# Optimization experiments

Hardware: AMD Instinct MI355X
Metric: run time of the kernel (lower is better)

## Reference

```python
import jax, jax.numpy as jnp
import numpy as np

B, T, D_MODEL, N_HEADS = 2, 2048, 2048, 16
D_HEAD = D_MODEL // N_HEADS
SCALE = 1.0 / np.sqrt(D_HEAD)


def setup_inputs() -> dict:
    key = jax.random.key(0)
    ks = jax.random.split(key, 5)
    w_std = 1.0 / np.sqrt(D_MODEL)
    x = jax.random.normal(ks[0], (B, T, D_MODEL), dtype=jnp.float32)
    W_q = jax.random.normal(ks[1], (D_MODEL, D_MODEL), dtype=jnp.float32) * w_std
    W_k = jax.random.normal(ks[2], (D_MODEL, D_MODEL), dtype=jnp.float32) * w_std
    W_v = jax.random.normal(ks[3], (D_MODEL, D_MODEL), dtype=jnp.float32) * w_std
    W_o = jax.random.normal(ks[4], (D_MODEL, D_MODEL), dtype=jnp.float32) * w_std
    return {"x": x, "W_q": W_q, "W_k": W_k, "W_v": W_v, "W_o": W_o}


def _split_heads(y):
    # [B, T, D] -> [B, H, T, d_head]
    b, t, _ = y.shape
    return y.reshape(b, t, N_HEADS, D_HEAD).transpose(0, 2, 1, 3)


def reference(x, W_q, W_k, W_v, W_o):
    # Linear layers (torch nn.Linear: y = x @ W.T)
    Q = _split_heads(x @ W_q.T)
    K = _split_heads(x @ W_k.T)
    V = _split_heads(x @ W_v.T)
    # Causal softmax attention (math-equivalent to the tiled online-softmax loop)
    scores = jnp.einsum('bhqd,bhkd->bhqk', Q, K) * SCALE
    causal_mask = jnp.tril(jnp.ones((T, T), dtype=bool))  # [T, T]
    scores = jnp.where(causal_mask, scores, -jnp.inf)
    P = jax.nn.softmax(scores, axis=-1)
    O = jnp.einsum('bhqk,bhkd->bhqd', P, V)
    out = O.transpose(0, 2, 1, 3).reshape(B, T, D_MODEL)  # merge heads
    return out @ W_o.T
```

## Files before the change

kernel.cpp:

```cpp
#include <hip/hip_runtime.h>
#include <hip/hip_bf16.h>
#include <hip/hip_fp16.h>

#define B_   2
#define T_   2048
#define DM   2048
#define NH   16
#define DH   128
#define M_   (B_*T_)
#define SCALE_ 0.08838834764831845f

typedef _Float16 f16;
typedef f16  half8 __attribute__((ext_vector_type(8)));
typedef f16  half4 __attribute__((ext_vector_type(4)));
typedef float f32x4 __attribute__((ext_vector_type(4)));

#define GL16(gp, lp) __builtin_amdgcn_global_load_lds( \
    (const __attribute__((address_space(1))) void*)(gp), \
    (__attribute__((address_space(3))) void*)(lp), 16, 0, 0)

#define MFMA16(a, b, c) __builtin_amdgcn_mfma_f32_16x16x32_f16((a), (b), (c), 0, 0, 0)

struct CvtArgs { const float* s[5]; f16* d[5]; };

__global__ __launch_bounds__(256) void convert_all(CvtArgs a) {
    size_t i4 = (size_t)blockIdx.x * 256 + threadIdx.x;
    int r; size_t off;
    if (i4 < 2097152) { r = 0; off = i4; }
    else { size_t k = i4 - 2097152; r = 1 + (int)(k >> 20); off = k & 1048575; }
    float4 v = *((const float4*)a.s[r] + off);
    half4 h;
    h[0] = (f16)v.x; h[1] = (f16)v.y; h[2] = (f16)v.z; h[3] = (f16)v.w;
    *((half4*)a.d[r] + off) = h;
}

#define NT_K 32

__global__ __launch_bounds__(512, 2)
void qkv3(const f16* __restrict__ A, const f16* __restrict__ Bw,
          f16* __restrict__ dst)
{
    __shared__ __align__(16) char smem[114688];

    const int tid  = threadIdx.x;
    const int lane = tid & 63;
    const int w    = tid >> 6;
    const int wr   = w >> 1, wc = w & 1;

    const int id = (blockIdx.x & 7) * 64 + (blockIdx.x >> 3);
    const int bm = id & 15, bn = id >> 4;
    const int m0 = bm * 256, n0 = bn * 192;

    const int scol8 = (((tid & 7) ^ ((tid >> 3) & 7)) << 3);
    const int rc0 = (((lane >> 4) * 16)      ) ^ ((lane & 7) << 4);
    const int rc1 = (64 + (lane >> 4) * 16   ) ^ ((lane & 7) << 4);

    f32x4 acc[4][6] = {};

#define QSTAGE_A(bufb, ch, s, kt) GL16( \
    A + (size_t)(m0 + (ch)*128 + (tid>>8)*64 + (s)*32 + ((tid>>3)&31)) * 2048 + (kt)*64 + scol8, \
    smem + (bufb)*57344 + (ch)*16384 + (s)*8192 + w*1024)
#define QSTAGE_B(bufb, u, kt) GL16( \
    Bw + (size_t)(n0 + (tid>>7)*48 + (u)*16 + ((tid>>3)&15)) * 2048 + (kt)*64 + scol8, \
    smem + (bufb)*57344 + 32768 + (u)*8192 + w*1024)

    const int abase = (wr >> 1) * 16384 + (wr & 1) * 4096 + (lane & 15) * 128;
    const int bbase = 32768 + wc * 4096 + (lane & 15) * 128;

    half8 af0[4][2], af1[4][2], bnx[2];

    QSTAGE_A(0, 0, 0, 0); QSTAGE_A(0, 0, 1, 0);
    QSTAGE_A(0, 1, 0, 0); QSTAGE_A(0, 1, 1, 0);
    QSTAGE_B(0, 0, 0);    QSTAGE_B(0, 1, 0);    QSTAGE_B(0, 2, 0);
    {
        asm volatile("s_waitcnt vmcnt(2)" ::: "memory");
        __builtin_amdgcn_s_barrier();
        __builtin_amdgcn_sched_barrier(0);
        const char* buf0 = smem;
        #pragma unroll
        for (int m = 0; m < 4; ++m) {
            const char* p = buf0 + (m >> 1) * 8192 + abase + (m & 1) * 2048;
            af0[m][0] = *(const half8*)(p + rc0);
            af0[m][1] = *(const half8*)(p + rc1);
        }
        bnx[0] = *(const half8*)(buf0 + bbase + rc0);
        bnx[1] = *(const half8*)(buf0 + bbase + rc1);
    }

#define GATE(n_) do { \
    asm volatile("s_waitcnt vmcnt(" #n_ ")" ::: "memory"); \
    __builtin_amdgcn_s_barrier(); \
    __builtin_amdgcn_sched_barrier(0); \
} while (0)

#define MFC(AF, BB, f_) do { \
    __builtin_amdgcn_s_setprio(1); \
    _Pragma("unroll") \
    for (int m_ = 0; m_ < 4; ++m_) { \
        acc[m_][f_] = MFMA16(AF[m_][0], (BB)[0], acc[m_][f_]); \
        acc[m_][f_] = MFMA16(AF[m_][1], (BB)[1], acc[m_][f_]); \
    } \
    __builtin_amdgcn_s_setprio(0); \
} while (0)

#define RDB(dstv, off) do { \
    const char* p_ = buf + bbase + (off); \
    dstv[0] = *(const half8*)(p_ + rc0); \
    dstv[1] = *(const half8*)(p_ + rc1); \
} while (0)

#define BODY(t_, c_, AFC, AFN) do { \
    const char* buf  = smem + (c_) * 57344; \
    const char* nbuf = smem + ((c_) ^ 1) * 57344; \
    const int  kt    = ((t_) + 1 < NT_K) ? (t_) + 1 : (t_); \
    half8 b3[2], b1[2], b4[2], b2[2], b5[2]; \
     \
    RDB(b3, 2048); \
    QSTAGE_A((c_) ^ 1, 0, 0, kt); QSTAGE_A((c_) ^ 1, 0, 1, kt); \
    MFC(AFC, bnx, 0); \
     \
    GATE(3); \
    RDB(b1, 8192); \
    QSTAGE_A((c_) ^ 1, 1, 0, kt); QSTAGE_A((c_) ^ 1, 1, 1, kt); \
    MFC(AFC, b3, 3); \
     \
    RDB(b4, 8192 + 2048); \
    QSTAGE_B((c_) ^ 1, 0, kt); \
    MFC(AFC, b1, 1); \
     \
    GATE(5); \
    RDB(b2, 16384); \
    QSTAGE_B((c_) ^ 1, 1, kt); \
    MFC(AFC, b4, 4); \
     \
    GATE(1); \
    RDB(b5, 16384 + 2048); \
    { const char* p_ = nbuf + abase; \
      AFN[0][0] = *(const half8*)(p_ + rc0); \
      AFN[0][1] = *(const half8*)(p_ + rc1); \
      AFN[1][0] = *(const half8*)(p_ + 2048 + rc0); \
      AFN[1][1] = *(const half8*)(p_ + 2048 + rc1); } \
    QSTAGE_B((c_) ^ 1, 2, kt); \
    MFC(AFC, b2, 2); \
     \
    { const char* p_ = nbuf + 8192 + abase; \
      AFN[2][0] = *(const half8*)(p_ + rc0); \
      AFN[2][1] = *(const half8*)(p_ + rc1); \
      AFN[3][0] = *(const half8*)(p_ + 2048 + rc0); \
      AFN[3][1] = *(const half8*)(p_ + 2048 + rc1); } \
    { const char* p_ = nbuf + bbase; \
      bnx[0] = *(const half8*)(p_ + rc0); \
      bnx[1] = *(const half8*)(p_ + rc1); } \
    MFC(AFC, b5, 5); \
} while (0)

    for (int t = 0; t < NT_K; t += 2) {
        BODY(t,     0, af0, af1);
        BODY(t + 1, 1, af1, af0);
    }
#undef BODY
#undef RDB
#undef MFC
#undef GATE
#undef QSTAGE_A
#undef QSTAGE_B

    asm volatile("s_waitcnt vmcnt(0)" ::: "memory");

    #pragma unroll
    for (int m = 0; m < 4; ++m)
        #pragma unroll
        for (int f = 0; f < 6; ++f)
            #pragma unroll
            for (int j = 0; j < 4; ++j) {
                int row  = m0 + wr * 64 + m * 16 + (lane >> 4) * 4 + j;
                int gcol = n0 + wc * 96 + f * 16 + (lane & 15);
                int sec = gcol >> 11, cic = gcol & 2047;
                int b = row >> 11, tt = row & (T_ - 1);
                int h = cic >> 7, d = cic & 127;
                float cs = (sec == 0) ? SCALE_ : 1.0f;
                dst[(size_t)sec * ((size_t)M_ * 2048) +
                    ((size_t)(b * NH + h) * T_ + tt) * DH + d] = (f16)(acc[m][f][j] * cs);
            }
}

__global__ __launch_bounds__(512, 4)
void wo2(const f16* __restrict__ A, const f16* __restrict__ Bw,
         float* __restrict__ Cf)
{
    __shared__ __align__(16) char smem[65536];

    const int tid  = threadIdx.x;
    const int lane = tid & 63;
    const int w    = tid >> 6;
    const int wr   = w >> 2, wc = w & 3;

    const int id = (blockIdx.x & 7) * 64 + (blockIdx.x >> 3);
    const int bm = id & 31, bn = id >> 5;
    const int m0 = bm * 128, n0 = bn * 128;

    const int scol8 = (((tid & 7) ^ ((tid >> 3) & 7)) << 3);
    const int rc0 = (((lane >> 4) * 16)      ) ^ ((lane & 7) << 4);
    const int rc1 = (64 + (lane >> 4) * 16   ) ^ ((lane & 7) << 4);

    f32x4 acc[4][2] = {};

#define WSTAGE_A(bufb, s, kt) GL16( \
    A + (size_t)(m0 + (tid>>8)*64 + (s)*32 + ((tid>>3)&31)) * 2048 + (kt)*64 + scol8, \
    smem + (bufb)*32768 + (s)*8192 + w*1024)
#define WSTAGE_B(bufb, u, kt) GL16( \
    Bw + (size_t)(n0 + (tid>>7)*32 + (u)*16 + ((tid>>3)&15)) * 2048 + (kt)*64 + scol8, \
    smem + (bufb)*32768 + 16384 + (u)*8192 + w*1024)

    WSTAGE_A(0, 0, 0); WSTAGE_A(0, 1, 0);
    WSTAGE_B(0, 0, 0); WSTAGE_B(0, 1, 0);

    const int abase = wr * 4096 + (lane & 15) * 128;
    const int bbase = 16384 + (wc * 16 + (lane & 15)) * 128;

    for (int t = 0; t < NT_K; ++t) {
        const int c  = t & 1;
        const char* buf = smem + c * 32768;
        const int kt = (t + 1 < NT_K) ? t + 1 : t;

        half8 af[4][2], bfr[2];
        asm volatile("s_waitcnt vmcnt(1)" ::: "memory");
        __builtin_amdgcn_s_barrier();
        __builtin_amdgcn_sched_barrier(0);
        #pragma unroll
        for (int m = 0; m < 4; ++m) {
            const char* p = buf + (m >> 1) * 8192 + abase + (m & 1) * 2048;
            af[m][0] = *(const half8*)(p + rc0);
            af[m][1] = *(const half8*)(p + rc1);
        }
        { const char* p = buf + bbase;
          bfr[0] = *(const half8*)(p + rc0); bfr[1] = *(const half8*)(p + rc1); }
        WSTAGE_A(c ^ 1, 0, kt); WSTAGE_A(c ^ 1, 1, kt);
        __builtin_amdgcn_s_setprio(1);
        #pragma unroll
        for (int m = 0; m < 4; ++m) {
            acc[m][0] = MFMA16(af[m][0], bfr[0], acc[m][0]);
            acc[m][0] = MFMA16(af[m][1], bfr[1], acc[m][0]);
        }
        __builtin_amdgcn_s_setprio(0);

        asm volatile("s_waitcnt vmcnt(2)" ::: "memory");
        __builtin_amdgcn_s_barrier();
        __builtin_amdgcn_sched_barrier(0);
        { const char* p = buf + bbase + 8192;
          bfr[0] = *(const half8*)(p + rc0); bfr[1] = *(const half8*)(p + rc1); }
        WSTAGE_B(c ^ 1, 0, kt); WSTAGE_B(c ^ 1, 1, kt);
        __builtin_amdgcn_s_setprio(1);
        #pragma unroll
        for (int m = 0; m < 4; ++m) {
            acc[m][1] = MFMA16(af[m][0], bfr[0], acc[m][1]);
            acc[m][1] = MFMA16(af[m][1], bfr[1], acc[m][1]);
        }
        __builtin_amdgcn_s_setprio(0);
        __builtin_amdgcn_s_barrier();
    }
#undef WSTAGE_A
#undef WSTAGE_B

    asm volatile("s_waitcnt vmcnt(0)" ::: "memory");

    #pragma unroll
    for (int m = 0; m < 4; ++m)
        #pragma unroll
        for (int u = 0; u < 2; ++u)
            #pragma unroll
            for (int j = 0; j < 4; ++j) {
                int row = m0 + wr * 64 + m * 16 + (lane >> 4) * 4 + j;
                int col = n0 + wc * 32 + u * 16 + (lane & 15);
                Cf[(size_t)row * 2048 + col] = acc[m][u][j];
            }
}

__global__ __launch_bounds__(256)
void vtrans(const f16* __restrict__ Vin, f16* __restrict__ Vout)
{
    __shared__ f16 ld[64][72];
    const int tid = threadIdx.x;
    const int dd = blockIdx.x;
    const int tt = blockIdx.y;
    const int bh = blockIdx.z;

    const int r  = tid >> 2;
    const int s2 = (tid & 3) * 2;

    const f16* src = Vin + ((size_t)bh * T_ + tt * 64 + r) * DH + dd * 64;
    half8 v0 = *(const half8*)(src + s2 * 8);
    half8 v1 = *(const half8*)(src + s2 * 8 + 8);
    #pragma unroll
    for (int e = 0; e < 8; ++e) ld[s2 * 8 + e][r]     = v0[e];
    #pragma unroll
    for (int e = 0; e < 8; ++e) ld[s2 * 8 + 8 + e][r] = v1[e];
    __syncthreads();

    f16* dst = Vout + ((size_t)bh * DH + dd * 64 + r) * T_ + tt * 64;
    *(half8*)(dst + s2 * 8)     = *(const half8*)&ld[r][s2 * 8];
    *(half8*)(dst + s2 * 8 + 8) = *(const half8*)&ld[r][s2 * 8 + 8];
}

#define QB 64
#define KB 64
#define PP 72
#define NQT (T_/QB)

__global__ __launch_bounds__(256, 4)
void attn_fwd(const f16* __restrict__ Q, const f16* __restrict__ K,
              const f16* __restrict__ Vt, f16* __restrict__ O)
{
    __shared__ __align__(16) char Ks[2][16384];
    __shared__ __align__(16) char Vs[2][16384];
    __shared__ __align__(16) f16 Ps[4][16][PP];

    const int tid  = threadIdx.x;
    const int lane = tid & 63;
    const int w    = tid >> 6;
    const int g    = lane >> 4;

    const int bid  = blockIdx.x;
    const int swz  = (bid & 7) * 64 + (bid >> 3);
    const int bh   = swz >> 4;
    const int pair = swz & 15;
    const size_t base = (size_t)bh * T_ * DH;
    const int b = bh >> 4, h = bh & 15;

    const int krow0 = w * 4 + g;
    const int kswz  = ((lane & 15) ^ (krow0 & 7)) << 3;
    const int vrow0 = w * 8 + (lane >> 3);
    const int vswz  = (((lane & 7) ^ ((lane >> 3) & 7)) << 3);

#define STAGE_K(c_, kv) do { \
    _Pragma("unroll") for (int i_ = 0; i_ < 4; ++i_) { \
        const f16* g_ = K + base + (size_t)((kv) + i_*16 + krow0) * DH + kswz; \
        GL16(g_, &Ks[c_][i_*4096 + w*1024]); } } while (0)
#define STAGE_V(c_, kv) do { \
    _Pragma("unroll") for (int i_ = 0; i_ < 4; ++i_) { \
        const f16* g_ = Vt + base + (size_t)(i_*32 + vrow0) * T_ + (kv) + vswz; \
        GL16(g_, &Vs[c_][i_*4096 + w*1024]); } } while (0)

    #pragma unroll
    for (int hf = 0; hf < 2; ++hf) {
        const int qt = (hf == 0) ? pair : (NQT - 1 - pair);
        const int q0 = qt * QB;
        const int ntiles = qt + 1;
        const int qg = q0 + w * 16 + (lane & 15);

        half8 qf[4];
        #pragma unroll
        for (int kk = 0; kk < 4; ++kk)
            qf[kk] = *reinterpret_cast<const half8*>(
                &Q[base + (size_t)qg * DH + kk * 32 + g * 8]);

        float mrun = -1e30f, lrun = 0.f;
        f32x4 o[8] = {};

        __syncthreads();
        STAGE_K(0, 0);
        STAGE_V(0, 0);

        for (int it = 0; it < ntiles; ++it) {
            const int c = it & 1;
            __syncthreads();
            if (it + 1 < ntiles) {
                STAGE_K(c ^ 1, (it + 1) * KB);
                STAGE_V(c ^ 1, (it + 1) * KB);
            }

            const char* kb = &Ks[c][0];
            f32x4 sacc[4] = {};
            __builtin_amdgcn_s_setprio(1);
            #pragma unroll
            for (int n = 0; n < 4; ++n)
                #pragma unroll
                for (int kk = 0; kk < 4; ++kk) {
                    half8 kfv = *(const half8*)(kb + (n*16 + (lane & 15)) * 256 +
                        ((kk*32 + g * 8) * 2 ^ ((lane & 7) << 4)));
                    sacc[n] = MFMA16(kfv, qf[kk], sacc[n]);
                }
            __builtin_amdgcn_s_setprio(0);

            if (it == ntiles - 1) {
                #pragma unroll
                for (int n = 0; n < 4; ++n)
                    #pragma unroll
                    for (int j = 0; j < 4; ++j) {
                        int kg = it * KB + n*16 + g*4 + j;
                        if (kg > qg) sacc[n][j] = -1e30f;
                    }
            }

            float mx = sacc[0][0];
            #pragma unroll
            for (int n = 0; n < 4; ++n)
                #pragma unroll
                for (int j = 0; j < 4; ++j) mx = fmaxf(mx, sacc[n][j]);
            mx = fmaxf(mx, __shfl_xor(mx, 16));
            mx = fmaxf(mx, __shfl_xor(mx, 32));
            float mnew = fmaxf(mrun, mx);
            float sf = __expf(mrun - mnew);
            float rs = 0.f;
            #pragma unroll
            for (int n = 0; n < 4; ++n)
                #pragma unroll
                for (int j = 0; j < 4; ++j) {
                    float p = __expf(sacc[n][j] - mnew);
                    sacc[n][j] = p;
                    rs += p;
                }
            rs += __shfl_xor(rs, 16);
            rs += __shfl_xor(rs, 32);
            lrun = lrun * sf + rs;
            mrun = mnew;
            #pragma unroll
            for (int nn = 0; nn < 8; ++nn) o[nn] *= sf;

            #pragma unroll
            for (int n = 0; n < 4; ++n) {
                half4 hv;
                hv[0] = (f16)sacc[n][0]; hv[1] = (f16)sacc[n][1];
                hv[2] = (f16)sacc[n][2]; hv[3] = (f16)sacc[n][3];
                *reinterpret_cast<half4*>(&Ps[w][lane & 15][n*16 + g*4]) = hv;
            }

            half8 bp[2];
            #pragma unroll
            for (int cc = 0; cc < 2; ++cc)
                bp[cc] = *reinterpret_cast<const half8*>(&Ps[w][lane & 15][cc*32 + g*8]);

            const char* vb = &Vs[c][0];
            __builtin_amdgcn_s_setprio(1);
            #pragma unroll
            for (int n = 0; n < 8; ++n)
                #pragma unroll
                for (int cc = 0; cc < 2; ++cc) {
                    half8 vf = *(const half8*)(vb + (n*16 + (lane & 15)) * 128 +
                        ((cc*64 + g*16) ^ ((lane & 7) << 4)));
                    o[n] = MFMA16(vf, bp[cc], o[n]);
                }
            __builtin_amdgcn_s_setprio(0);
        }

        float invl = 1.0f / lrun;
        #pragma unroll
        for (int n = 0; n < 8; ++n) {
            half4 hv;
            hv[0] = (f16)(o[n][0] * invl); hv[1] = (f16)(o[n][1] * invl);
            hv[2] = (f16)(o[n][2] * invl); hv[3] = (f16)(o[n][3] * invl);
            *reinterpret_cast<half4*>(
                &O[((size_t)(b * T_ + qg) * NH + h) * DH + n*16 + g*4]) = hv;
        }
    }
#undef STAGE_K
#undef STAGE_V
}

extern "C" void kernel_launch(void* const* d_in, const int* in_sizes, int n_in,
                              void* d_out, int out_size, void* d_ws, size_t ws_size,
                              hipStream_t stream)
{
    const float* x  = (const float*)d_in[0];
    const float* wq = (const float*)d_in[1];
    const float* wk = (const float*)d_in[2];
    const float* wv = (const float*)d_in[3];
    const float* wo = (const float*)d_in[4];
    float* out = (float*)d_out;

    const size_t nx = (size_t)M_ * DM;
    const size_t nw = (size_t)DM * DM;
    const size_t need = (nx * 5 + nw * 4) * sizeof(f16);
    if (ws_size < need) return;

    char* ws = (char*)d_ws;
    f16* xh  = (f16*)ws;  ws += nx * 2;
    f16* wqh = (f16*)ws;  ws += nw * 2;
    f16* wkh = (f16*)ws;  ws += nw * 2;
    f16* wvh = (f16*)ws;  ws += nw * 2;
    f16* woh = (f16*)ws;  ws += nw * 2;
    f16* Qh  = (f16*)ws;  ws += nx * 2;
    f16* Kh  = (f16*)ws;  ws += nx * 2;
    f16* Vh  = (f16*)ws;  ws += nx * 2;
    f16* Oh  = (f16*)ws;  ws += nx * 2;

    f16* Vth = xh;

    CvtArgs ca;
    ca.s[0] = x;  ca.d[0] = xh;
    ca.s[1] = wq; ca.d[1] = wqh;
    ca.s[2] = wk; ca.d[2] = wkh;
    ca.s[3] = wv; ca.d[3] = wvh;
    ca.s[4] = wo; ca.d[4] = woh;
    convert_all<<<24576, 256, 0, stream>>>(ca);

    qkv3<<<dim3(512), 512, 0, stream>>>(xh, wqh, Qh);

    vtrans<<<dim3(2, 32, 32), 256, 0, stream>>>(Vh, Vth);

    attn_fwd<<<dim3(512), 256, 0, stream>>>(Qh, Kh, Vth, Oh);

    wo2<<<dim3(512), 512, 0, stream>>>(Oh, woh, out);
}
```

Baseline: 234.4 us.

## Process both paired query tiles in one K/V sweep in attention

The attention kernel used to handle its two paired query tiles (early and late) one after the other, loading K/V twice. It now sweeps the K/V tiles once for both, so each staged K/V tile serves two sets of MFMAs while the early tile is still active. This doubles the accumulator registers, so launch bounds drop to 2 blocks per SM. The wo2 loop count also changes from NT_K to a new NT_W constant of 32, which may or may not equal the old value.

Result: no change. 236.4 us (+0.8%).

```diff
diff --git a/kernel.cpp b/kernel.cpp
--- a/kernel.cpp
+++ b/kernel.cpp
@@ -184,6 +184,8 @@
             }
 }
 
+#define NT_W 32
+
 __global__ __launch_bounds__(512, 4)
 void wo2(const f16* __restrict__ A, const f16* __restrict__ Bw,
          float* __restrict__ Cf)
@@ -218,10 +220,10 @@
     const int abase = wr * 4096 + (lane & 15) * 128;
     const int bbase = 16384 + (wc * 16 + (lane & 15)) * 128;
 
-    for (int t = 0; t < NT_K; ++t) {
+    for (int t = 0; t < NT_W; ++t) {
         const int c  = t & 1;
         const char* buf = smem + c * 32768;
-        const int kt = (t + 1 < NT_K) ? t + 1 : t;
+        const int kt = (t + 1 < NT_W) ? t + 1 : t;
 
         half8 af[4][2], bfr[2];
         asm volatile("s_waitcnt vmcnt(1)" ::: "memory");
@@ -307,7 +309,7 @@
 #define PP 72
 #define NQT (T_/QB)
 
-__global__ __launch_bounds__(256, 4)
+__global__ __launch_bounds__(256, 2)
 void attn_fwd(const f16* __restrict__ Q, const f16* __restrict__ K,
               const f16* __restrict__ Vt, f16* __restrict__ O)
 {
@@ -341,116 +343,209 @@
         const f16* g_ = Vt + base + (size_t)(i_*32 + vrow0) * T_ + (kv) + vswz; \
         GL16(g_, &Vs[c_][i_*4096 + w*1024]); } } while (0)
 
+    const int qt1 = pair;
+    const int qt2 = NQT - 1 - pair;
+    const int nt1 = qt1 + 1;
+    const int ntU = qt2 + 1;
+    const int qg1 = qt1 * QB + w * 16 + (lane & 15);
+    const int qg2 = qt2 * QB + w * 16 + (lane & 15);
+
+    half8 qf1[4], qf2[4];
     #pragma unroll
-    for (int hf = 0; hf < 2; ++hf) {
-        const int qt = (hf == 0) ? pair : (NQT - 1 - pair);
-        const int q0 = qt * QB;
-        const int ntiles = qt + 1;
-        const int qg = q0 + w * 16 + (lane & 15);
-
-        half8 qf[4];
-        #pragma unroll
-        for (int kk = 0; kk < 4; ++kk)
-            qf[kk] = *reinterpret_cast<const half8*>(
-                &Q[base + (size_t)qg * DH + kk * 32 + g * 8]);
-
-        float mrun = -1e30f, lrun = 0.f;
-        f32x4 o[8] = {};
-
+    for (int kk = 0; kk < 4; ++kk) {
+        qf1[kk] = *reinterpret_cast<const half8*>(
+            &Q[base + (size_t)qg1 * DH + kk * 32 + g * 8]);
+        qf2[kk] = *reinterpret_cast<const half8*>(
+            &Q[base + (size_t)qg2 * DH + kk * 32 + g * 8]);
+    }
+
+    float mrun1 = -1e30f, lrun1 = 0.f;
+    float mrun2 = -1e30f, lrun2 = 0.f;
+    f32x4 o1[8] = {};
+    f32x4 o2[8] = {};
+
+    STAGE_K(0, 0);
+    STAGE_V(0, 0);
+
+    for (int it = 0; it < ntU; ++it) {
+        const int c = it & 1;
         __syncthreads();
-        STAGE_K(0, 0);
-        STAGE_V(0, 0);
-
-        for (int it = 0; it < ntiles; ++it) {
-            const int c = it & 1;
-            __syncthreads();
-            if (it + 1 < ntiles) {
-                STAGE_K(c ^ 1, (it + 1) * KB);
-                STAGE_V(c ^ 1, (it + 1) * KB);
-            }
-
-            const char* kb = &Ks[c][0];
-            f32x4 sacc[4] = {};
-            __builtin_amdgcn_s_setprio(1);
+        if (it + 1 < ntU) {
+            STAGE_K(c ^ 1, (it + 1) * KB);
+            STAGE_V(c ^ 1, (it + 1) * KB);
+        }
+        const bool s1 = (it < nt1);
+
+        const char* kb = &Ks[c][0];
+        f32x4 sa1[4] = {};
+        f32x4 sa2[4] = {};
+        __builtin_amdgcn_s_setprio(1);
+        if (s1) {
             #pragma unroll
             for (int n = 0; n < 4; ++n)
                 #pragma unroll
                 for (int kk = 0; kk < 4; ++kk) {
                     half8 kfv = *(const half8*)(kb + (n*16 + (lane & 15)) * 256 +
                         ((kk*32 + g * 8) * 2 ^ ((lane & 7) << 4)));
-                    sacc[n] = MFMA16(kfv, qf[kk], sacc[n]);
-                }
-            __builtin_amdgcn_s_setprio(0);
-
-            if (it == ntiles - 1) {
-                #pragma unroll
-                for (int n = 0; n < 4; ++n)
-                    #pragma unroll
-                    for (int j = 0; j < 4; ++j) {
-                        int kg = it * KB + n*16 + g*4 + j;
-                        if (kg > qg) sacc[n][j] = -1e30f;
-                    }
-            }
-
-            float mx = sacc[0][0];
-            #pragma unroll
-            for (int n = 0; n < 4; ++n)
-                #pragma unroll
-                for (int j = 0; j < 4; ++j) mx = fmaxf(mx, sacc[n][j]);
+                    sa2[n] = MFMA16(kfv, qf2[kk], sa2[n]);
+                    sa1[n] = MFMA16(kfv, qf1[kk], sa1[n]);
+                }
+        } else {
+            #pragma unroll
+            for (int n = 0; n < 4; ++n)
+                #pragma unroll
+                for (int kk = 0; kk < 4; ++kk) {
+                    half8 kfv = *(const half8*)(kb + (n*16 + (lane & 15)) * 256 +
+                        ((kk*32 + g * 8) * 2 ^ ((lane & 7) << 4)));
+                    sa2[n] = MFMA16(kfv, qf2[kk], sa2[n]);
+                }
+        }
+        __builtin_amdgcn_s_setprio(0);
+
+        if (it == ntU - 1) {
+            #pragma unroll
+            for (int n = 0; n < 4; ++n)
+                #pragma unroll
+                for (int j = 0; j < 4; ++j) {
+                    int kg = it * KB + n*16 + g*4 + j;
+                    if (kg > qg2) sa2[n][j] = -1e30f;
+                }
+        }
+        if (s1 && it == nt1 - 1) {
+            #pragma unroll
+            for (int n = 0; n < 4; ++n)
+                #pragma unroll
+                for (int j = 0; j < 4; ++j) {
+                    int kg = it * KB + n*16 + g*4 + j;
+                    if (kg > qg1) sa1[n][j] = -1e30f;
+                }
+        }
+
+        float sf1 = 1.f, sf2;
+        {
+            float mx = sa2[0][0];
+            #pragma unroll
+            for (int n = 0; n < 4; ++n)
+                #pragma unroll
+                for (int j = 0; j < 4; ++j) mx = fmaxf(mx, sa2[n][j]);
             mx = fmaxf(mx, __shfl_xor(mx, 16));
             mx = fmaxf(mx, __shfl_xor(mx, 32));
-            float mnew = fmaxf(mrun, mx);
-            float sf = __expf(mrun - mnew);
+            float mnew = fmaxf(mrun2, mx);
+            sf2 = __expf(mrun2 - mnew);
             float rs = 0.f;
             #pragma unroll
             for (int n = 0; n < 4; ++n)
                 #pragma unroll
                 for (int j = 0; j < 4; ++j) {
-                    float p = __expf(sacc[n][j] - mnew);
-                    sacc[n][j] = p;
+                    float p = __expf(sa2[n][j] - mnew);
+                    sa2[n][j] = p;
                     rs += p;
                 }
             rs += __shfl_xor(rs, 16);
             rs += __shfl_xor(rs, 32);
-            lrun = lrun * sf + rs;
-            mrun = mnew;
-            #pragma unroll
-            for (int nn = 0; nn < 8; ++nn) o[nn] *= sf;
-
+            lrun2 = lrun2 * sf2 + rs;
+            mrun2 = mnew;
+        }
+        if (s1) {
+            float mx = sa1[0][0];
+            #pragma unroll
+            for (int n = 0; n < 4; ++n)
+                #pragma unroll
+                for (int j = 0; j < 4; ++j) mx = fmaxf(mx, sa1[n][j]);
+            mx = fmaxf(mx, __shfl_xor(mx, 16));
+            mx = fmaxf(mx, __shfl_xor(mx, 32));
+            float mnew = fmaxf(mrun1, mx);
+            sf1 = __expf(mrun1 - mnew);
+            float rs = 0.f;
+            #pragma unroll
+            for (int n = 0; n < 4; ++n)
+                #pragma unroll
+                for (int j = 0; j < 4; ++j) {
+                    float p = __expf(sa1[n][j] - mnew);
+                    sa1[n][j] = p;
+                    rs += p;
+                }
+            rs += __shfl_xor(rs, 16);
+            rs += __shfl_xor(rs, 32);
+            lrun1 = lrun1 * sf1 + rs;
+            mrun1 = mnew;
+        }
+        #pragma unroll
+        for (int nn = 0; nn < 8; ++nn) o2[nn] *= sf2;
+        if (s1) {
+            #pragma unroll
+            for (int nn = 0; nn < 8; ++nn) o1[nn] *= sf1;
+        }
+
+        half8 bp1[2], bp2[2];
+        if (s1) {
             #pragma unroll
             for (int n = 0; n < 4; ++n) {
                 half4 hv;
-                hv[0] = (f16)sacc[n][0]; hv[1] = (f16)sacc[n][1];
-                hv[2] = (f16)sacc[n][2]; hv[3] = (f16)sacc[n][3];
+                hv[0] = (f16)sa1[n][0]; hv[1] = (f16)sa1[n][1];
+                hv[2] = (f16)sa1[n][2]; hv[3] = (f16)sa1[n][3];
                 *reinterpret_cast<half4*>(&Ps[w][lane & 15][n*16 + g*4]) = hv;
             }
-
-            half8 bp[2];
             #pragma unroll
             for (int cc = 0; cc < 2; ++cc)
-                bp[cc] = *reinterpret_cast<const half8*>(&Ps[w][lane & 15][cc*32 + g*8]);
-
-            const char* vb = &Vs[c][0];
-            __builtin_amdgcn_s_setprio(1);
+                bp1[cc] = *reinterpret_cast<const half8*>(&Ps[w][lane & 15][cc*32 + g*8]);
+        }
+        #pragma unroll
+        for (int n = 0; n < 4; ++n) {
+            half4 hv;
+            hv[0] = (f16)sa2[n][0]; hv[1] = (f16)sa2[n][1];
+            hv[2] = (f16)sa2[n][2]; hv[3] = (f16)sa2[n][3];
+            *reinterpret_cast<half4*>(&Ps[w][lane & 15][n*16 + g*4]) = hv;
+        }
+        #pragma unroll
+        for (int cc = 0; cc < 2; ++cc)
+            bp2[cc] = *reinterpret_cast<const half8*>(&Ps[w][lane & 15][cc*32 + g*8]);
+
+        const char* vb = &Vs[c][0];
+        __builtin_amdgcn_s_setprio(1);
+        if (s1) {
             #pragma unroll
             for (int n = 0; n < 8; ++n)
                 #pragma unroll
                 for (int cc = 0; cc < 2; ++cc) {
                     half8 vf = *(const half8*)(vb + (n*16 + (lane & 15)) * 128 +
                         ((cc*64 + g*16) ^ ((lane & 7) << 4)));
-                    o[n] = MFMA16(vf, bp[cc], o[n]);
-                }
-            __builtin_amdgcn_s_setprio(0);
-        }
-
-        float invl = 1.0f / lrun;
+                    o2[n] = MFMA16(vf, bp2[cc], o2[n]);
+                    o1[n] = MFMA16(vf, bp1[cc], o1[n]);
+                }
+        } else {
+            #pragma unroll
+            for (int n = 0; n < 8; ++n)
+                #pragma unroll
+                for (int cc = 0; cc < 2; ++cc) {
+                    half8 vf = *(const half8*)(vb + (n*16 + (lane & 15)) * 128 +
+                        ((cc*64 + g*16) ^ ((lane & 7) << 4)));
+                    o2[n] = MFMA16(vf, bp2[cc], o2[n]);
+                }
+        }
+        __builtin_amdgcn_s_setprio(0);
+    }
+
+    {
+        float invl = 1.0f / lrun2;
         #pragma unroll
         for (int n = 0; n < 8; ++n) {
             half4 hv;
-            hv[0] = (f16)(o[n][0] * invl); hv[1] = (f16)(o[n][1] * invl);
-            hv[2] = (f16)(o[n][2] * invl); hv[3] = (f16)(o[n][3] * invl);
+            hv[0] = (f16)(o2[n][0] * invl); hv[1] = (f16)(o2[n][1] * invl);
+            hv[2] = (f16)(o2[n][2] * invl); hv[3] = (f16)(o2[n][3] * invl);
             *reinterpret_cast<half4*>(
-                &O[((size_t)(b * T_ + qg) * NH + h) * DH + n*16 + g*4]) = hv;
+                &O[((size_t)(b * T_ + qg2) * NH + h) * DH + n*16 + g*4]) = hv;
+        }
+    }
+    {
+        float invl = 1.0f / lrun1;
+        #pragma unroll
+        for (int n = 0; n < 8; ++n) {
+            half4 hv;
+            hv[0] = (f16)(o1[n][0] * invl); hv[1] = (f16)(o1[n][1] * invl);
+            hv[2] = (f16)(o1[n][2] * invl); hv[3] = (f16)(o1[n][3] * invl);
+            *reinterpret_cast<half4*>(
+                &O[((size_t)(b * T_ + qg1) * NH + h) * DH + n*16 + g*4]) = hv;
         }
     }
 #undef STAGE_K
```

## Fuse paired query tiles into one KV loop with lazy softmax rescaling

Applied to the files above, without the earlier changes.

The attention kernel now handles both query tiles of a causal pair in a single pass over K/V. Each staged K/V tile is reused by both tiles instead of being loaded twice. Softmax rescaling is skipped unless the running max grows by more than a threshold, and the row-sum reduction is deferred to the end. Launch bounds drop to 2 blocks per SM because of higher register pressure, and the wo2 loop count gets its own constant. The trade-off is lower occupancy and a lazy-rescale approach that assumes bounded score growth.

New measurement: 232.9 us. About the same (-0.7%).

```diff
diff --git a/kernel.cpp b/kernel.cpp
--- a/kernel.cpp
+++ b/kernel.cpp
@@ -184,6 +184,8 @@
             }
 }
 
+#define NT_W 32
+
 __global__ __launch_bounds__(512, 4)
 void wo2(const f16* __restrict__ A, const f16* __restrict__ Bw,
          float* __restrict__ Cf)
@@ -218,10 +220,10 @@
     const int abase = wr * 4096 + (lane & 15) * 128;
     const int bbase = 16384 + (wc * 16 + (lane & 15)) * 128;
 
-    for (int t = 0; t < NT_K; ++t) {
+    for (int t = 0; t < NT_W; ++t) {
         const int c  = t & 1;
         const char* buf = smem + c * 32768;
-        const int kt = (t + 1 < NT_K) ? t + 1 : t;
+        const int kt = (t + 1 < NT_W) ? t + 1 : t;
 
         half8 af[4][2], bfr[2];
         asm volatile("s_waitcnt vmcnt(1)" ::: "memory");
@@ -307,7 +309,7 @@
 #define PP 72
 #define NQT (T_/QB)
 
-__global__ __launch_bounds__(256, 4)
+__global__ __launch_bounds__(256, 2)
 void attn_fwd(const f16* __restrict__ Q, const f16* __restrict__ K,
               const f16* __restrict__ Vt, f16* __restrict__ O)
 {
@@ -341,118 +343,178 @@
         const f16* g_ = Vt + base + (size_t)(i_*32 + vrow0) * T_ + (kv) + vswz; \
         GL16(g_, &Vs[c_][i_*4096 + w*1024]); } } while (0)
 
+#define QKT(SA, QF) do { \
+    __builtin_amdgcn_s_setprio(1); \
+    _Pragma("unroll") \
+    for (int n_ = 0; n_ < 4; ++n_) \
+        _Pragma("unroll") \
+        for (int kk_ = 0; kk_ < 4; ++kk_) { \
+            half8 kfv = *(const half8*)(kb + (n_*16 + (lane & 15)) * 256 + \
+                ((kk_*32 + g * 8) * 2 ^ ((lane & 7) << 4))); \
+            SA[n_] = MFMA16(kfv, QF[kk_], SA[n_]); \
+        } \
+    __builtin_amdgcn_s_setprio(0); \
+} while (0)
+
+#define SMAX(SA, MRUN, LSUM, OO) do { \
+    float mx_ = SA[0][0]; \
+    _Pragma("unroll") \
+    for (int n_ = 0; n_ < 4; ++n_) \
+        _Pragma("unroll") \
+        for (int j_ = 0; j_ < 4; ++j_) mx_ = fmaxf(mx_, SA[n_][j_]); \
+    mx_ = fmaxf(mx_, __shfl_xor(mx_, 16)); \
+    mx_ = fmaxf(mx_, __shfl_xor(mx_, 32)); \
+    if (!__all(mx_ <= MRUN + 5.f)) { \
+        float mnew_ = fmaxf(MRUN, mx_); \
+        float sf_ = __expf(MRUN - mnew_); \
+        _Pragma("unroll") \
+        for (int nn_ = 0; nn_ < 8; ++nn_) OO[nn_] *= sf_; \
+        LSUM *= sf_; \
+        MRUN = mnew_; \
+    } \
+    float rs_ = 0.f; \
+    _Pragma("unroll") \
+    for (int n_ = 0; n_ < 4; ++n_) \
+        _Pragma("unroll") \
+        for (int j_ = 0; j_ < 4; ++j_) { \
+            float p_ = __expf(SA[n_][j_] - MRUN); \
+            SA[n_][j_] = p_; \
+            rs_ += p_; \
+        } \
+    LSUM += rs_; \
+} while (0)
+
+#define PFRAG(SA, BP) do { \
+    _Pragma("unroll") \
+    for (int n_ = 0; n_ < 4; ++n_) { \
+        half4 hv_; \
+        hv_[0] = (f16)SA[n_][0]; hv_[1] = (f16)SA[n_][1]; \
+        hv_[2] = (f16)SA[n_][2]; hv_[3] = (f16)SA[n_][3]; \
+        *reinterpret_cast<half4*>(&Ps[w][lane & 15][n_*16 + g*4]) = hv_; \
+    } \
+    _Pragma("unroll") \
+    for (int cc_ = 0; cc_ < 2; ++cc_) \
+        BP[cc_] = *reinterpret_cast<const half8*>(&Ps[w][lane & 15][cc_*32 + g*8]); \
+} while (0)
+
+#define PV(OO, BP) do { \
+    __builtin_amdgcn_s_setprio(1); \
+    _Pragma("unroll") \
+    for (int n_ = 0; n_ < 8; ++n_) \
+        _Pragma("unroll") \
+        for (int cc_ = 0; cc_ < 2; ++cc_) { \
+            half8 vf_ = *(const half8*)(vb + (n_*16 + (lane & 15)) * 128 + \
+                ((cc_*64 + g*16) ^ ((lane & 7) << 4))); \
+            OO[n_] = MFMA16(vf_, BP[cc_], OO[n_]); \
+        } \
+    __builtin_amdgcn_s_setprio(0); \
+} while (0)
+
+    const int qt1 = pair;
+    const int qt2 = NQT - 1 - pair;
+    const int nt1 = qt1 + 1;
+    const int ntU = qt2 + 1;
+    const int qg1 = qt1 * QB + w * 16 + (lane & 15);
+    const int qg2 = qt2 * QB + w * 16 + (lane & 15);
+
+    half8 qf1[4], qf2[4];
     #pragma unroll
-    for (int hf = 0; hf < 2; ++hf) {
-        const int qt = (hf == 0) ? pair : (NQT - 1 - pair);
-        const int q0 = qt * QB;
-        const int ntiles = qt + 1;
-        const int qg = q0 + w * 16 + (lane & 15);
-
-        half8 qf[4];
-        #pragma unroll
-        for (int kk = 0; kk < 4; ++kk)
-            qf[kk] = *reinterpret_cast<const half8*>(
-                &Q[base + (size_t)qg * DH + kk * 32 + g * 8]);
-
-        float mrun = -1e30f, lrun = 0.f;
-        f32x4 o[8] = {};
-
+    for (int kk = 0; kk < 4; ++kk) {
+        qf1[kk] = *reinterpret_cast<const half8*>(
+            &Q[base + (size_t)qg1 * DH + kk * 32 + g * 8]);
+        qf2[kk] = *reinterpret_cast<const half8*>(
+            &Q[base + (size_t)qg2 * DH + kk * 32 + g * 8]);
+    }
+
+    float mrun1 = -1e30f, lsum1 = 0.f;
+    float mrun2 = -1e30f, lsum2 = 0.f;
+    f32x4 o1[8] = {};
+    f32x4 o2[8] = {};
+
+    STAGE_K(0, 0);
+    STAGE_V(0, 0);
+
+    for (int it = 0; it < ntU; ++it) {
+        const int c = it & 1;
         __syncthreads();
-        STAGE_K(0, 0);
-        STAGE_V(0, 0);
-
-        for (int it = 0; it < ntiles; ++it) {
-            const int c = it & 1;
-            __syncthreads();
-            if (it + 1 < ntiles) {
-                STAGE_K(c ^ 1, (it + 1) * KB);
-                STAGE_V(c ^ 1, (it + 1) * KB);
-            }
-
-            const char* kb = &Ks[c][0];
-            f32x4 sacc[4] = {};
-            __builtin_amdgcn_s_setprio(1);
-            #pragma unroll
-            for (int n = 0; n < 4; ++n)
-                #pragma unroll
-                for (int kk = 0; kk < 4; ++kk) {
-                    half8 kfv = *(const half8*)(kb + (n*16 + (lane & 15)) * 256 +
-                        ((kk*32 + g * 8) * 2 ^ ((lane & 7) << 4)));
-                    sacc[n] = MFMA16(kfv, qf[kk], sacc[n]);
-                }
-            __builtin_amdgcn_s_setprio(0);
-
-            if (it == ntiles - 1) {
-                #pragma unroll
-                for (int n = 0; n < 4; ++n)
-                    #pragma unroll
-                    for (int j = 0; j < 4; ++j) {
-                        int kg = it * KB + n*16 + g*4 + j;
-                        if (kg > qg) sacc[n][j] = -1e30f;
-                    }
-            }
-
-            float mx = sacc[0][0];
-            #pragma unroll
-            for (int n = 0; n < 4; ++n)
-                #pragma unroll
-                for (int j = 0; j < 4; ++j) mx = fmaxf(mx, sacc[n][j]);
-            mx = fmaxf(mx, __shfl_xor(mx, 16));
-            mx = fmaxf(mx, __shfl_xor(mx, 32));
-            float mnew = fmaxf(mrun, mx);
-            float sf = __expf(mrun - mnew);
-            float rs = 0.f;
+        if (it + 1 < ntU) {
+            STAGE_K(c ^ 1, (it + 1) * KB);
+            STAGE_V(c ^ 1, (it + 1) * KB);
+        }
+        const bool s1 = (it < nt1);
+        const char* kb = &Ks[c][0];
+        const char* vb = &Vs[c][0];
+
+        f32x4 sa2[4] = {};
+        f32x4 sa1[4] = {};
+
+        QKT(sa2, qf2);
+        if (s1) QKT(sa1, qf1);
+
+        if (it == ntU - 1) {
             #pragma unroll
             for (int n = 0; n < 4; ++n)
                 #pragma unroll
                 for (int j = 0; j < 4; ++j) {
-                    float p = __expf(sacc[n][j] - mnew);
-                    sacc[n][j] = p;
-                    rs += p;
+                    int kg = it * KB + n*16 + g*4 + j;
+                    if (kg > qg2) sa2[n][j] = -1e30f;
                 }
-            rs += __shfl_xor(rs, 16);
-            rs += __shfl_xor(rs, 32);
-            lrun = lrun * sf + rs;
-            mrun = mnew;
+        }
+        if (s1 && it == nt1 - 1) {
             #pragma unroll
-            for (int nn = 0; nn < 8; ++nn) o[nn] *= sf;
-
-            #pragma unroll
-            for (int n = 0; n < 4; ++n) {
-                half4 hv;
-                hv[0] = (f16)sacc[n][0]; hv[1] = (f16)sacc[n][1];
-                hv[2] = (f16)sacc[n][2]; hv[3] = (f16)sacc[n][3];
-                *reinterpret_cast<half4*>(&Ps[w][lane & 15][n*16 + g*4]) = hv;
-            }
-
-            half8 bp[2];
-            #pragma unroll
-            for (int cc = 0; cc < 2; ++cc)
-                bp[cc] = *reinterpret_cast<const half8*>(&Ps[w][lane & 15][cc*32 + g*8]);
-
-            const char* vb = &Vs[c][0];
-            __builtin_amdgcn_s_setprio(1);
-            #pragma unroll
-            for (int n = 0; n < 8; ++n)
+            for (int n = 0; n < 4; ++n)
                 #pragma unroll
-                for (int cc = 0; cc < 2; ++cc) {
-                    half8 vf = *(const half8*)(vb + (n*16 + (lane & 15)) * 128 +
-                        ((cc*64 + g*16) ^ ((lane & 7) << 4)));
-                    o[n] = MFMA16(vf, bp[cc], o[n]);
+                for (int j = 0; j < 4; ++j) {
+                    int kg = it * KB + n*16 + g*4 + j;
+                    if (kg > qg1) sa1[n][j] = -1e30f;
                 }
-            __builtin_amdgcn_s_setprio(0);
-        }
-
-        float invl = 1.0f / lrun;
+        }
+
+        SMAX(sa2, mrun2, lsum2, o2);
+        half8 bp2[2];
+        PFRAG(sa2, bp2);
+        PV(o2, bp2);
+
+        if (s1) {
+            SMAX(sa1, mrun1, lsum1, o1);
+            half8 bp1[2];
+            PFRAG(sa1, bp1);
+            PV(o1, bp1);
+        }
+    }
+
+    {
+        float l2 = lsum2;
+        l2 += __shfl_xor(l2, 16);
+        l2 += __shfl_xor(l2, 32);
+        float invl = 1.0f / l2;
         #pragma unroll
         for (int n = 0; n < 8; ++n) {
             half4 hv;
-            hv[0] = (f16)(o[n][0] * invl); hv[1] = (f16)(o[n][1] * invl);
-            hv[2] = (f16)(o[n][2] * invl); hv[3] = (f16)(o[n][3] * invl);
+            hv[0] = (f16)(o2[n][0] * invl); hv[1] = (f16)(o2[n][1] * invl);
+            hv[2] = (f16)(o2[n][2] * invl); hv[3] = (f16)(o2[n][3] * invl);
             *reinterpret_cast<half4*>(
-                &O[((size_t)(b * T_ + qg) * NH + h) * DH + n*16 + g*4]) = hv;
-        }
-    }
+                &O[((size_t)(b * T_ + qg2) * NH + h) * DH + n*16 + g*4]) = hv;
+        }
+    }
+    {
+        float l1 = lsum1;
+        l1 += __shfl_xor(l1, 16);
+        l1 += __shfl_xor(l1, 32);
+        float invl = 1.0f / l1;
+        #pragma unroll
+        for (int n = 0; n < 8; ++n) {
+            half4 hv;
+            hv[0] = (f16)(o1[n][0] * invl); hv[1] = (f16)(o1[n][1] * invl);
+            hv[2] = (f16)(o1[n][2] * invl); hv[3] = (f16)(o1[n][3] * invl);
+            *reinterpret_cast<half4*>(
+                &O[((size_t)(b * T_ + qg1) * NH + h) * DH + n*16 + g*4]) = hv;
+        }
+    }
+#undef PV
+#undef PFRAG
+#undef SMAX
+#undef QKT
 #undef STAGE_K
 #undef STAGE_V
 }
```
